# Kernel tuning notes

Measured on AMD Instinct MI355X. Metric: run time of the kernel, lower is better.

## Reference

```python
import jax, jax.numpy as jnp
import numpy as np
from jax import lax

SIGMA = 0.8
THRESH_MIN = 50.0
THRESH_MAX = 80.0
TRACK_CONN = 5
TRACK_ITERS = 3


def _gaussian_kernel(sigma=SIGMA):
    ks = int(((sigma - 0.8) / 0.3 + 1) * 2 + 1)
    ks += 1 if ks % 2 == 0 else 0
    ax = np.arange(-ks // 2 + 1.0, ks // 2 + 1.0)
    xx, yy = np.meshgrid(ax, ax)
    normal = 1 / (2.0 * np.pi * sigma ** 2)
    k = np.exp(-(xx ** 2 + yy ** 2) / (2.0 * sigma ** 2)) * normal
    k = k / np.sum(k)
    return k.reshape(ks, ks, 1, 1).astype(np.float32)


def _sobel_kernel():
    gx = np.array([[-1, 0, 1], [-2, 0, 2], [-1, 0, 1]], dtype=np.float32)
    gy = np.array([[1, 2, 1], [0, 0, 0], [-1, -2, -1]], dtype=np.float32)
    return np.stack([gx, gy], axis=-1).reshape(3, 3, 1, 2)


def setup_inputs() -> dict:
    key = jax.random.key(0)
    x = jax.random.uniform(key, (8, 1024, 1024, 1), dtype=jnp.float32) * 255.0
    return {
        'x': x,
        'gaussian_kernel': jnp.asarray(_gaussian_kernel()),
        'sobel_kernel': jnp.asarray(_sobel_kernel()),
    }


def _conv_same(x, k):
    return lax.conv_general_dilated(x, k, (1, 1), 'SAME',
                                    dimension_numbers=('NHWC', 'HWIO', 'NHWC'))


# offsets with kernel value 0 (others are -inf) for the 4 angle NMS kernels
_ANGLE_OFFSETS = [
    [(0, -1), (0, 0), (0, 1)],     # 0 deg
    [(-1, 1), (0, 0), (1, -1)],    # 45 deg
    [(-1, 0), (0, 0), (1, 0)],     # 90 deg
    [(-1, -1), (0, 0), (1, 1)],    # 135 deg
]


def _angle_dilation(ar):
    # morphological dilation (tf.nn.dilation2d) with -inf masked 3x3 kernels,
    # realized as max over the 3 unmasked shifts per angle channel.
    B, H, W, _ = ar.shape
    pad = jnp.pad(ar, ((0, 0), (1, 1), (1, 1), (0, 0)),
                  constant_values=-jnp.inf)
    outs = []
    for c, offs in enumerate(_ANGLE_OFFSETS):
        ch = pad[..., c]
        m = ch[:, 1 + offs[0][0]:1 + offs[0][0] + H, 1 + offs[0][1]:1 + offs[0][1] + W]
        for dy, dx in offs[1:]:
            m = jnp.maximum(m, ch[:, 1 + dy:1 + dy + H, 1 + dx:1 + dx + W])
        outs.append(m)
    return jnp.stack(outs, axis=-1)


def _canny(x, gaussian_kernel, sobel_kernel):
    dt = x.dtype
    x_smooth = _conv_same(x, gaussian_kernel)
    grad_xy = _conv_same(x_smooth, sobel_kernel)
    gx, gy = grad_xy[..., 0:1], grad_xy[..., 1:2]
    theta = (jnp.arctan2(gy, gx) * (180.0 / np.pi) + 90.0) % 180.0
    grad_mag = jnp.clip(jnp.sqrt(gx * gx + gy * gy), 0.0, 255.0)

    # angle-bucketed masks (channels: 0, 45, 90, 135 deg)
    m0 = (theta >= 157.5) | (theta <= 22.5)
    m1 = (theta >= 22.5) & (theta < 67.5)
    m2 = (theta >= 67.5) & (theta < 112.5)
    m3 = (theta >= 112.5) & (theta < 157.5)
    masks = jnp.concatenate([m0, m1, m2, m3], axis=-1).astype(dt)
    angle_responses = masks * grad_mag  # (B,H,W,4)

    max_pool_angle = _angle_dilation(angle_responses)

    # non-max suppression + double threshold
    suppressed = jnp.where(max_pool_angle == angle_responses, grad_mag, 0.0)
    edge_candidates = jnp.max(suppressed, axis=-1, keepdims=True)
    strong = (edge_candidates >= THRESH_MAX).astype(dt)
    weak = ((edge_candidates >= THRESH_MIN) & (edge_candidates < THRESH_MAX)).astype(dt)

    # iterative hysteresis: weak pixels adjacent (within KxK window) to strong
    # pixels become strong
    win = (1, TRACK_CONN, TRACK_CONN, 1)
    for _ in range(TRACK_ITERS):
        pooled = lax.reduce_window(strong, -jnp.inf, lax.max, win,
                                   (1, 1, 1, 1), 'SAME')
        strong = jnp.clip(strong + weak * pooled, 0.0, 1.0)
    return strong.astype(dt)


def reference(x, gaussian_kernel, sobel_kernel):
    return _canny(x, gaussian_kernel, sobel_kernel)
```

## Files before the change

### kernel.cpp

```cpp
#include <hip/hip_runtime.h>
#include <math.h>

#define NT   1024
#define TS   64
#define HX   9
#define XR   82
#define XSTR 84
#define ST   80
#define SSTR 84
#define MT   78
#define MSTR 80
#define WT   76
#define WPR  3
#define HB   6

#define POOLA 31200

template<bool IN>
__device__ __forceinline__ void canny_tile(
    const float* __restrict__ xb, const float* __restrict__ g,
    float* __restrict__ ob, int H, int W, int ty0, int tx0, int tid,
    float* __restrict__ s_x, float* __restrict__ s_mag,
    unsigned char* __restrict__ s_dirb, float* __restrict__ s_sm,
    unsigned char* __restrict__ s_byte, unsigned int* __restrict__ s_bsA,
    unsigned int* __restrict__ s_bsB, unsigned int* __restrict__ s_bw)
{
  for (int i = tid; i < XR*XSTR; i += NT) {
    int r = i / XSTR, c = i - r*XSTR;
    int gy = ty0 + r - HX, gx = tx0 + c - HX;
    float v = 0.f;
    if (IN || ((unsigned)gy < (unsigned)H && (unsigned)gx < (unsigned)W))
      v = xb[(size_t)gy*W + gx];
    s_x[i] = v;
  }
  __syncthreads();

  if (tid < 800) {
    int qr = tid / 20, qc = tid - qr*20;
    int r0 = 2*qr, c0 = 4*qc;
    float xq[4][6];
#pragma unroll
    for (int j = 0; j < 4; ++j) {
      const float* xr = &s_x[(r0+j)*XSTR + c0];
      float4 a = *(const float4*)xr;
      float2 bq = *(const float2*)(xr+4);
      xq[j][0]=a.x; xq[j][1]=a.y; xq[j][2]=a.z; xq[j][3]=a.w;
      xq[j][4]=bq.x; xq[j][5]=bq.y;
    }
#pragma unroll
    for (int ry = 0; ry < 2; ++ry) {
      float o[4];
#pragma unroll
      for (int k = 0; k < 4; ++k) {
        int gy = ty0 + (r0+ry) - (HX-1), gx = tx0 + (c0+k) - (HX-1);
        float acc = 0.f;
        if (IN || ((unsigned)gy < (unsigned)H && (unsigned)gx < (unsigned)W)) {
#pragma unroll
          for (int dy = 0; dy < 3; ++dy)
#pragma unroll
            for (int dx = 0; dx < 3; ++dx)
              acc += xq[ry+dy][k+dx] * g[dy*3+dx];
        }
        o[k] = acc;
      }
      *(float4*)&s_sm[(r0+ry)*SSTR + c0] = make_float4(o[0],o[1],o[2],o[3]);
    }
  } else if (tid < 880) {
    int r = tid - 800;
    *(float4*)&s_sm[r*SSTR + ST] = make_float4(0.f,0.f,0.f,0.f);
  }
  __syncthreads();

  if (tid < 780) {
    int qr = tid / 20, qc = tid - qr*20;
    int r0 = 2*qr, c0 = 4*qc;
    float sq[4][6];
#pragma unroll
    for (int j = 0; j < 4; ++j) {
      const float* sr = &s_sm[(r0+j)*SSTR + c0];
      float4 a = *(const float4*)sr;
      float2 bq = *(const float2*)(sr+4);
      sq[j][0]=a.x; sq[j][1]=a.y; sq[j][2]=a.z; sq[j][3]=a.w;
      sq[j][4]=bq.x; sq[j][5]=bq.y;
    }
#pragma unroll
    for (int ry = 0; ry < 2; ++ry) {
      float mg[4]; unsigned int dw = 0;
#pragma unroll
      for (int k = 0; k < 4; ++k) {
        float a00=sq[ry][k],   a01=sq[ry][k+1],   a02=sq[ry][k+2];
        float a10=sq[ry+1][k],                    a12=sq[ry+1][k+2];
        float a20=sq[ry+2][k], a21=sq[ry+2][k+1], a22=sq[ry+2][k+2];
        float mag = 0.f; unsigned int dir = 0;
        int gy = ty0 + (r0+ry) - (HX-2), gx = tx0 + (c0+k) - (HX-2);
        if (IN || ((unsigned)gy < (unsigned)H && (unsigned)gx < (unsigned)W)) {
          float fgx = 0.f - a00;
          fgx += a02;
          fgx = fmaf(a10, -2.f, fgx);
          fgx = fmaf(a12,  2.f, fgx);
          fgx -= a20;
          fgx += a22;
          float fgy = a00;
          fgy = fmaf(a01, 2.f, fgy);
          fgy += a02;
          fgy -= a20;
          fgy = fmaf(a21, -2.f, fgy);
          fgy -= a22;
          mag = fminf(sqrtf(fgx*fgx + fgy*fgy), 255.f);
          float ax = fabsf(fgx), ay = fabsf(fgy);
          float sum = ax + ay;
          float d1 = ay - 0.41421356237f*ax;
          float d2 = ay - 2.41421356237f*ax;
          float band = 1e-4f * sum;
          if (sum == 0.f) {
            dir = 4;
          } else if (fabsf(d1) >= band && fabsf(d2) >= band) {
            if (d2 > 0.f)      dir = 1;
            else if (d1 < 0.f) dir = 4;
            else dir = (((__float_as_uint(fgx) ^ __float_as_uint(fgy)) >> 31) & 1)
                         ? 2 : 8;
          } else {
            float th = atan2f(fgy, fgx) * 57.29577951308232f + 90.0f;
            if (th < 0.f) th += 180.f; else if (th >= 180.f) th -= 180.f;
            if (th >= 157.5f || th <= 22.5f)  dir |= 1;
            if (th >= 22.5f  && th < 67.5f)   dir |= 2;
            if (th >= 67.5f  && th < 112.5f)  dir |= 4;
            if (th >= 112.5f && th < 157.5f)  dir |= 8;
          }
        }
        mg[k] = mag;
        dw |= dir << (8*k);
      }
      *(float4*)&s_mag[(r0+ry)*MSTR + c0] = make_float4(mg[0],mg[1],mg[2],mg[3]);
      *(unsigned int*)&s_dirb[(r0+ry)*MSTR + c0] = dw;
    }
  }
  __syncthreads();

  if (tid < 722) {
    int qr = tid / 19, qc = tid - qr*19;
    int r0 = 2*qr, c0 = 4*qc;
    float mq[4][6]; unsigned long long dq[4];
#pragma unroll
    for (int j = 0; j < 4; ++j) {
      const float* mr = &s_mag[(r0+j)*MSTR + c0];
      float4 a = *(const float4*)mr;
      float2 bq = *(const float2*)(mr+4);
      mq[j][0]=a.x; mq[j][1]=a.y; mq[j][2]=a.z; mq[j][3]=a.w;
      mq[j][4]=bq.x; mq[j][5]=bq.y;
      const unsigned char* dr = &s_dirb[(r0+j)*MSTR + c0];
      dq[j] = (unsigned long long)(*(const unsigned int*)dr)
            | ((unsigned long long)(*(const unsigned short*)(dr+4)) << 32);
    }
#pragma unroll
    for (int ry = 0; ry < 2; ++ry) {
      unsigned int outw = 0;
      unsigned long long d0 = dq[ry], d1 = dq[ry+1], d2 = dq[ry+2];
#pragma unroll
      for (int k = 0; k < 4; ++k) {
        float mag = mq[ry+1][k+1];
        unsigned int dc = (unsigned int)(d1 >> (8*(k+1))) & 0xFu;
        bool keep = false;
        {
          float rp = (dc & 1) ? mag : 0.f;
          float a  = ((d1 >> (8*k))     & 1) ? mq[ry+1][k]   : 0.f;
          float bb = ((d1 >> (8*(k+2))) & 1) ? mq[ry+1][k+2] : 0.f;
          keep = keep || (a <= rp && bb <= rp);
        }
        {
          float rp = (dc & 2) ? mag : 0.f;
          float a  = ((d0 >> (8*(k+2))) & 2) ? mq[ry][k+2]   : 0.f;
          float bb = ((d2 >> (8*k))     & 2) ? mq[ry+2][k]   : 0.f;
          keep = keep || (a <= rp && bb <= rp);
        }
        {
          float rp = (dc & 4) ? mag : 0.f;
          float a  = ((d0 >> (8*(k+1))) & 4) ? mq[ry][k+1]   : 0.f;
          float bb = ((d2 >> (8*(k+1))) & 4) ? mq[ry+2][k+1] : 0.f;
          keep = keep || (a <= rp && bb <= rp);
        }
        {
          float rp = (dc & 8) ? mag : 0.f;
          float a  = ((d0 >> (8*k))     & 8) ? mq[ry][k]     : 0.f;
          float bb = ((d2 >> (8*(k+2))) & 8) ? mq[ry+2][k+2] : 0.f;
          keep = keep || (a <= rp && bb <= rp);
        }
        unsigned int v = keep ? ((mag >= 80.f) ? 2u : ((mag >= 50.f) ? 1u : 0u)) : 0u;
        outw |= v << (8*k);
      }
      *(unsigned int*)&s_byte[(r0+ry)*WT + c0] = outw;
    }
  }
  __syncthreads();

  if (tid < WT*WPR) {
    int r = tid / WPR, k = tid - r*WPR;
    const unsigned char* row = &s_byte[r*WT + 32*k];
    int nw = (k < 2) ? 8 : 3;
    unsigned int sb = 0, wb = 0;
#pragma unroll
    for (int q = 0; q < 8; ++q) {
      if (q < nw) {
        unsigned int w = *(const unsigned int*)(row + 4*q);
        unsigned int t = (w >> 1) & 0x01010101u;
        unsigned int u = w & 0x01010101u;
        sb |= (((t * 0x01020408u) >> 24) & 0xFu) << (4*q);
        wb |= (((u * 0x01020408u) >> 24) & 0xFu) << (4*q);
      }
    }
    s_bsA[tid] = sb;
    s_bsB[tid] = sb;
    s_bw[tid]  = wb;
  }
  __syncthreads();

#pragma unroll
  for (int it = 0; it < 3; ++it) {
    const unsigned int* src = (it == 1) ? s_bsB : s_bsA;
    unsigned int*       dst = (it == 1) ? s_bsA : s_bsB;
    if (tid < (WT-4)*WPR) {
      int r = tid / WPR + 2, k = tid - (r-2)*WPR;
      unsigned int p = 0, selfw = 0;
#pragma unroll
      for (int dr = 0; dr < 5; ++dr) {
        int row = r - 2 + dr;
        unsigned int s  = src[row*WPR + k];
        unsigned int lo = (k > 0)     ? src[row*WPR + k - 1] : 0u;
        unsigned int hi = (k < WPR-1) ? src[row*WPR + k + 1] : 0u;
        p |= s | (s<<1) | (s<<2) | (s>>1) | (s>>2)
               | (lo>>30) | (lo>>31) | (hi<<30) | (hi<<31);
        if (dr == 2) selfw = s;
      }
      dst[r*WPR + k] = selfw | (s_bw[r*WPR + k] & p);
    }
    __syncthreads();
  }

  if (IN) {
    int r = tid >> 4, mq = tid & 15;
    int cc0 = 4*mq + HB;
    int rr = r + HB;
    int k0 = cc0 >> 5;
    unsigned long long wp = (unsigned long long)s_bsB[rr*WPR + k0]
                          | ((unsigned long long)s_bsB[rr*WPR + k0 + 1] << 32);
    unsigned int bits = (unsigned int)(wp >> (cc0 & 31));
    float4 o;
    o.x = (float)(bits & 1u);
    o.y = (float)((bits >> 1) & 1u);
    o.z = (float)((bits >> 2) & 1u);
    o.w = (float)((bits >> 3) & 1u);
    *(float4*)&ob[(size_t)(ty0+r)*W + tx0 + 4*mq] = o;
  } else {
    for (int i = tid; i < TS*TS; i += NT) {
      int r = i / TS, c = i - r*TS;
      int oy = ty0 + r, ox = tx0 + c;
      if (oy < H && ox < W) {
        int rr = r + HB, cc = c + HB;
        unsigned int w = s_bsB[rr*WPR + (cc >> 5)];
        ob[(size_t)oy*W + ox] = (float)((w >> (cc & 31)) & 1u);
      }
    }
  }
}

__global__ __launch_bounds__(NT, 8) void canny_fused(
    const float* __restrict__ x, const float* __restrict__ gk,
    float* __restrict__ out, int H, int W, int tilesX, int tilesY)
{
  __shared__ __align__(16) unsigned char poolA[POOLA];
  float* s_x   = (float*)poolA;
  float* s_mag = (float*)poolA;
  unsigned char* s_dirb = poolA + MT*MSTR*4;
  __shared__ __align__(16) float s_sm[ST*SSTR];
  unsigned char* s_byte = (unsigned char*)s_sm;
  unsigned int* s_bsA = (unsigned int*)((unsigned char*)s_sm + 5792);
  unsigned int* s_bsB = s_bsA + WT*WPR;
  unsigned int* s_bw  = s_bsB + WT*WPR;

  const int tpi = tilesX * tilesY;
  const int b  = blockIdx.x / tpi;
  const int t  = blockIdx.x % tpi;
  const int ty0 = (t / tilesX) * TS;
  const int tx0 = (t % tilesX) * TS;
  const float* xb = x + (size_t)b * H * W;
  float* ob = out + (size_t)b * H * W;
  const int tid = threadIdx.x;

  float g[9];
#pragma unroll
  for (int i = 0; i < 9; ++i) g[i] = gk[i];

  const bool interior = (ty0 >= HX) && (ty0 + XR - HX <= H)
                     && (tx0 >= HX) && (tx0 + XSTR - HX <= W);
  if (interior)
    canny_tile<true >(xb, g, ob, H, W, ty0, tx0, tid,
                      s_x, s_mag, s_dirb, s_sm, s_byte, s_bsA, s_bsB, s_bw);
  else
    canny_tile<false>(xb, g, ob, H, W, ty0, tx0, tid,
                      s_x, s_mag, s_dirb, s_sm, s_byte, s_bsA, s_bsB, s_bw);
}

extern "C" void kernel_launch(void* const* d_in, const int* in_sizes, int n_in,
                              void* d_out, int out_size, void* d_ws, size_t ws_size,
                              hipStream_t stream)
{
  const float* x  = (const float*)d_in[0];
  const float* gk = (const float*)d_in[1];
  float* out = (float*)d_out;

  const int H = 1024, W = 1024;
  const int B = in_sizes[0] / (H * W);
  const int tilesX = (W + TS - 1) / TS, tilesY = (H + TS - 1) / TS;

  dim3 grid(B * tilesX * tilesY);
  canny_fused<<<grid, NT, 0, stream>>>(x, gk, out, H, W, tilesX, tilesY);
}
```

Before: 140.1 us.

## Pack NMS strong/weak bits directly via LDS atomics and drop byte-pack stage

The NMS stage now writes strong and weak bitmasks straight into the packed bit arrays with LDS atomicOr, removing the intermediate byte buffer, one extra pass and one barrier. The zeroing of the bit arrays is done by otherwise idle threads in the gradient stage, and border rows of the ping-pong buffer are copied during the first hysteresis iteration. The global-to-LDS load is restructured into a fixed 7-step unrolled loop per thread, avoiding per-element div/mod. The keep test uses fmaxf instead of two comparisons. The cost is LDS atomics and an additional separate shared allocation.

```diff
diff --git a/kernel.cpp b/kernel.cpp
--- a/kernel.cpp
+++ b/kernel.cpp
@@ -22,16 +22,25 @@
     float* __restrict__ ob, int H, int W, int ty0, int tx0, int tid,
     float* __restrict__ s_x, float* __restrict__ s_mag,
     unsigned char* __restrict__ s_dirb, float* __restrict__ s_sm,
-    unsigned char* __restrict__ s_byte, unsigned int* __restrict__ s_bsA,
-    unsigned int* __restrict__ s_bsB, unsigned int* __restrict__ s_bw)
+    unsigned int* __restrict__ s_bsA, unsigned int* __restrict__ s_bsB,
+    unsigned int* __restrict__ s_bw)
 {
-  for (int i = tid; i < XR*XSTR; i += NT) {
-    int r = i / XSTR, c = i - r*XSTR;
-    int gy = ty0 + r - HX, gx = tx0 + c - HX;
-    float v = 0.f;
-    if (IN || ((unsigned)gy < (unsigned)H && (unsigned)gx < (unsigned)W))
-      v = xb[(size_t)gy*W + gx];
-    s_x[i] = v;
+  {
+    int c  = tid % XSTR;
+    int r0 = tid / XSTR;
+    float* dst = s_x + r0*XSTR + c;
+    const float* src = xb + (size_t)(ty0 + r0 - HX)*W + (tx0 + c - HX);
+    const bool cok = IN || ((unsigned)(tx0 + c - HX) < (unsigned)W);
+    int r = r0;
+#pragma unroll
+    for (int k = 0; k < 7; ++k) {
+      if (r < XR) {
+        float v = 0.f;
+        if (IN || (cok && (unsigned)(ty0 + r - HX) < (unsigned)H)) v = *src;
+        *dst = v;
+      }
+      r += 12; dst += 12*XSTR; src += (size_t)12*W;
+    }
   }
   __syncthreads();
 
@@ -134,6 +143,10 @@
       *(float4*)&s_mag[(r0+ry)*MSTR + c0] = make_float4(mg[0],mg[1],mg[2],mg[3]);
       *(unsigned int*)&s_dirb[(r0+ry)*MSTR + c0] = dw;
     }
+  } else if (tid < 780 + WT*WPR) {
+    int z = tid - 780;
+    s_bsA[z] = 0u;
+    s_bw[z]  = 0u;
   }
   __syncthreads();
 
@@ -154,7 +167,7 @@
     }
 #pragma unroll
     for (int ry = 0; ry < 2; ++ry) {
-      unsigned int outw = 0;
+      unsigned int sbn = 0, wbn = 0;
       unsigned long long d0 = dq[ry], d1 = dq[ry+1], d2 = dq[ry+2];
 #pragma unroll
       for (int k = 0; k < 4; ++k) {
@@ -165,52 +178,36 @@
           float rp = (dc & 1) ? mag : 0.f;
           float a  = ((d1 >> (8*k))     & 1) ? mq[ry+1][k]   : 0.f;
           float bb = ((d1 >> (8*(k+2))) & 1) ? mq[ry+1][k+2] : 0.f;
-          keep = keep || (a <= rp && bb <= rp);
+          keep = keep || (fmaxf(a, bb) <= rp);
         }
         {
           float rp = (dc & 2) ? mag : 0.f;
           float a  = ((d0 >> (8*(k+2))) & 2) ? mq[ry][k+2]   : 0.f;
           float bb = ((d2 >> (8*k))     & 2) ? mq[ry+2][k]   : 0.f;
-          keep = keep || (a <= rp && bb <= rp);
+          keep = keep || (fmaxf(a, bb) <= rp);
         }
         {
           float rp = (dc & 4) ? mag : 0.f;
           float a  = ((d0 >> (8*(k+1))) & 4) ? mq[ry][k+1]   : 0.f;
           float bb = ((d2 >> (8*(k+1))) & 4) ? mq[ry+2][k+1] : 0.f;
-          keep = keep || (a <= rp && bb <= rp);
+          keep = keep || (fmaxf(a, bb) <= rp);
         }
         {
           float rp = (dc & 8) ? mag : 0.f;
           float a  = ((d0 >> (8*k))     & 8) ? mq[ry][k]     : 0.f;
           float bb = ((d2 >> (8*(k+2))) & 8) ? mq[ry+2][k+2] : 0.f;
-          keep = keep || (a <= rp && bb <= rp);
-        }
-        unsigned int v = keep ? ((mag >= 80.f) ? 2u : ((mag >= 50.f) ? 1u : 0u)) : 0u;
-        outw |= v << (8*k);
-      }
-      *(unsigned int*)&s_byte[(r0+ry)*WT + c0] = outw;
-    }
-  }
-  __syncthreads();
-
-  if (tid < WT*WPR) {
-    int r = tid / WPR, k = tid - r*WPR;
-    const unsigned char* row = &s_byte[r*WT + 32*k];
-    int nw = (k < 2) ? 8 : 3;
-    unsigned int sb = 0, wb = 0;
-#pragma unroll
-    for (int q = 0; q < 8; ++q) {
-      if (q < nw) {
-        unsigned int w = *(const unsigned int*)(row + 4*q);
-        unsigned int t = (w >> 1) & 0x01010101u;
-        unsigned int u = w & 0x01010101u;
-        sb |= (((t * 0x01020408u) >> 24) & 0xFu) << (4*q);
-        wb |= (((u * 0x01020408u) >> 24) & 0xFu) << (4*q);
-      }
-    }
-    s_bsA[tid] = sb;
-    s_bsB[tid] = sb;
-    s_bw[tid]  = wb;
+          keep = keep || (fmaxf(a, bb) <= rp);
+        }
+        unsigned int sbit = (keep && mag >= 80.f) ? 1u : 0u;
+        unsigned int wbit = (keep && mag >= 50.f && mag < 80.f) ? 1u : 0u;
+        sbn |= sbit << k;
+        wbn |= wbit << k;
+      }
+      int word = (r0+ry)*WPR + (c0 >> 5);
+      int sh   = c0 & 31;
+      atomicOr(&s_bsA[word], sbn << sh);
+      atomicOr(&s_bw[word],  wbn << sh);
+    }
   }
   __syncthreads();
 
@@ -232,6 +229,12 @@
         if (dr == 2) selfw = s;
       }
       dst[r*WPR + k] = selfw | (s_bw[r*WPR + k] & p);
+    } else if (it == 0 && tid < (WT-4)*WPR + 12) {
+      int w = tid - (WT-4)*WPR;
+      int q = w / 3;
+      int row = (q < 2) ? q : 72 + q;
+      int k = w - q*3;
+      s_bsB[row*WPR + k] = s_bsA[row*WPR + k];
     }
     __syncthreads();
   }
@@ -272,10 +275,10 @@
   float* s_mag = (float*)poolA;
   unsigned char* s_dirb = poolA + MT*MSTR*4;
   __shared__ __align__(16) float s_sm[ST*SSTR];
-  unsigned char* s_byte = (unsigned char*)s_sm;
-  unsigned int* s_bsA = (unsigned int*)((unsigned char*)s_sm + 5792);
-  unsigned int* s_bsB = s_bsA + WT*WPR;
-  unsigned int* s_bw  = s_bsB + WT*WPR;
+  __shared__ __align__(16) unsigned int s_bits[3*WT*WPR];
+  unsigned int* s_bsA = s_bits;
+  unsigned int* s_bsB = s_bits + WT*WPR;
+  unsigned int* s_bw  = s_bits + 2*WT*WPR;
 
   const int tpi = tilesX * tilesY;
   const int b  = blockIdx.x / tpi;
@@ -294,10 +297,10 @@
                      && (tx0 >= HX) && (tx0 + XSTR - HX <= W);
   if (interior)
     canny_tile<true >(xb, g, ob, H, W, ty0, tx0, tid,
-                      s_x, s_mag, s_dirb, s_sm, s_byte, s_bsA, s_bsB, s_bw);
+                      s_x, s_mag, s_dirb, s_sm, s_bsA, s_bsB, s_bw);
   else
     canny_tile<false>(xb, g, ob, H, W, ty0, tx0, tid,
-                      s_x, s_mag, s_dirb, s_sm, s_byte, s_bsA, s_bsB, s_bw);
+                      s_x, s_mag, s_dirb, s_sm, s_bsA, s_bsB, s_bw);
 }
 
 extern "C" void kernel_launch(void* const* d_in, const int* in_sizes, int n_in,
```

Measured after the change: 136.4 us. 2.6% less time.
